# Performance work log

Measured on AMD Instinct MI355X. Metric: run time of the kernel, lower is better.

The kernel has to match this reference:

```python
import jax, jax.numpy as jnp
import numpy as np

EPS = 1e-5  # torch BatchNorm1d default eps

def _bn(x, g, b, m, v):
    # eval-mode BatchNorm1d with running statistics
    return (x - m) * jax.lax.rsqrt(v + EPS) * g + b

def setup_inputs() -> dict:
    key = jax.random.key(0)
    ks = jax.random.split(key, 6)
    N, E, D = 10000, 320000, 128
    h = jax.random.normal(ks[0], (N, D), dtype=jnp.float32)
    src = jax.random.randint(ks[1], (E,), 0, N)
    dst = jax.random.randint(ks[2], (E,), 0, N)
    # Linear weights (torch layout: [out, in]), kaiming-ish scale
    W0 = jax.random.normal(ks[3], (128, 256), dtype=jnp.float32) * (1.0 / np.sqrt(256))
    b0 = jnp.zeros((128,), jnp.float32)
    W1 = jax.random.normal(ks[4], (128, 128), dtype=jnp.float32) * (1.0 / np.sqrt(128))
    b1 = jnp.zeros((128,), jnp.float32)
    W2 = jax.random.normal(ks[5], (1, 128), dtype=jnp.float32) * (1.0 / np.sqrt(128))
    b2 = jnp.zeros((1,), jnp.float32)
    # BatchNorm affine params + running stats per layer input size
    g0, be0, m0, v0 = jnp.ones((256,)), jnp.zeros((256,)), jnp.zeros((256,)), jnp.ones((256,))
    g1, be1, m1, v1 = jnp.ones((128,)), jnp.zeros((128,)), jnp.zeros((128,)), jnp.ones((128,))
    g2, be2, m2, v2 = jnp.ones((128,)), jnp.zeros((128,)), jnp.zeros((128,)), jnp.ones((128,))
    return dict(h=h, src=src, dst=dst, W0=W0, b0=b0, W1=W1, b1=b1, W2=W2, b2=b2,
                g0=g0, be0=be0, g1=g1, be1=be1, g2=g2, be2=be2,
                m0=m0, v0=v0, m1=m1, v1=v1, m2=m2, v2=v2)

def reference(h, src, dst, W0, b0, W1, b1, W2, b2,
              g0, be0, g1, be1, g2, be2, m0, v0, m1, v1, m2, v2):
    # edge gather + concat: [E, 2*D]
    x = jnp.concatenate([h[src], h[dst]], axis=1)
    # stage 0: BN -> Linear (dropout is identity in eval)
    x = _bn(x, g0, be0, m0, v0) @ W0.T + b0
    # stage 1: ReLU -> BN -> Linear
    x = jax.nn.relu(x)
    x = _bn(x, g1, be1, m1, v1) @ W1.T + b1
    # stage 2: ReLU -> BN -> Linear
    x = jax.nn.relu(x)
    x = _bn(x, g2, be2, m2, v2) @ W2.T + b2
    return x  # [E, 1] edge scores
```

## Files before the change

kernel.cpp:

```cpp
#include <hip/hip_runtime.h>
#include <hip/hip_bf16.h>

#define BN_EPS 1e-5f
#define MG 2
#define GEDGES 32

typedef short bf16x8 __attribute__((ext_vector_type(8)));
typedef float f32x4  __attribute__((ext_vector_type(4)));

static __device__ __forceinline__ unsigned short f2bf(float f) {
    union { float f; unsigned int u; } v; v.f = f;
    unsigned int u = v.u;
    unsigned int r = (u + 0x7FFFu + ((u >> 16) & 1u)) >> 16;
    return (unsigned short)r;
}

static __device__ __forceinline__ unsigned short f2bf_hw(float f) {
    __hip_bfloat16 b = __float2bfloat16(f);
    union { __hip_bfloat16 b; unsigned short u; } v; v.b = b;
    return v.u;
}

static __device__ __forceinline__ unsigned short f2h(float f) {
    union { _Float16 h; unsigned short u; } v; v.h = (_Float16)f;
    return v.u;
}

static __device__ __forceinline__ float h2f(short s) {
    union { short s; _Float16 h; } v; v.s = s;
    return (float)v.h;
}

__global__ __launch_bounds__(256) void k_prep(
        const float* __restrict__ h, unsigned short* __restrict__ hb, int n4, int nCvt,
        const float* __restrict__ W0, const float* __restrict__ b0,
        const float* __restrict__ W1, const float* __restrict__ b1,
        const float* __restrict__ W2, const float* __restrict__ b2,
        const float* __restrict__ g0, const float* __restrict__ be0,
        const float* __restrict__ m0, const float* __restrict__ v0,
        const float* __restrict__ g1, const float* __restrict__ be1,
        const float* __restrict__ m1, const float* __restrict__ v1,
        const float* __restrict__ g2, const float* __restrict__ be2,
        const float* __restrict__ m2, const float* __restrict__ v2,
        unsigned short* __restrict__ W0sw, unsigned short* __restrict__ W1sw,
        float* __restrict__ b0f, float* __restrict__ b1f,
        float* __restrict__ w2f, float* __restrict__ b2f) {
    const int b = blockIdx.x;
    const int tid = threadIdx.x;

    if (b < nCvt) {
        int i = b * 256 + tid;
        if (i < n4) {
            float4 f = ((const float4*)h)[i];
            ushort4 o;
            o.x = f2bf(f.x); o.y = f2bf(f.y); o.z = f2bf(f.z); o.w = f2bf(f.w);
            ((ushort4*)hb)[i] = o;
        }
        return;
    }
    int br = b - nCvt;
    if (br < 128) {
        int t = br * 256 + tid;
        int j = t & 7, lane = (t >> 3) & 63, nt = (t >> 9) & 7, kb = t >> 12;
        int k = kb * 32 + (lane >> 4) * 8 + j;
        int n = nt * 16 + (lane & 15);
        float s = g0[k] * rsqrtf(v0[k] + BN_EPS);
        W0sw[t] = f2bf(W0[n * 256 + k] * s);
        return;
    }
    br -= 128;
    if (br < 64) {
        int t = br * 256 + tid;
        int j = t & 7, lane = (t >> 3) & 63, nt = (t >> 9) & 7, kb = t >> 12;
        int k = kb * 32 + (lane >> 4) * 8 + j;
        int n = nt * 16 + (lane & 15);
        float s = g1[k] * rsqrtf(v1[k] + BN_EPS);
        W1sw[t] = f2bf(W1[n * 128 + k] * s);
        return;
    }
    br -= 64;
    {
        if (tid >= 64) return;
        const int i = br, lane = tid;
        float s0 = 0.f;
#pragma unroll
        for (int c = 0; c < 4; c++) {
            int k = c * 64 + lane;
            float sc = g0[k] * rsqrtf(v0[k] + BN_EPS);
            s0 += W0[i * 256 + k] * (be0[k] - m0[k] * sc);
        }
        float s1 = 0.f;
#pragma unroll
        for (int c = 0; c < 2; c++) {
            int k = c * 64 + lane;
            float sc = g1[k] * rsqrtf(v1[k] + BN_EPS);
            s1 += W1[i * 128 + k] * (be1[k] - m1[k] * sc);
        }
        float s2 = 0.f;
        if (i == 0) {
#pragma unroll
            for (int c = 0; c < 2; c++) {
                int k = c * 64 + lane;
                float sc = g2[k] * rsqrtf(v2[k] + BN_EPS);
                s2 += W2[k] * (be2[k] - m2[k] * sc);
            }
        }
#pragma unroll
        for (int off = 1; off < 64; off <<= 1) {
            s0 += __shfl_xor(s0, off);
            s1 += __shfl_xor(s1, off);
            s2 += __shfl_xor(s2, off);
        }
        if (lane == 0) {
            b0f[i] = b0[i] + s0;
            b1f[i] = b1[i] + s1;
            w2f[i] = W2[i] * (g2[i] * rsqrtf(v2[i] + BN_EPS));
            if (i == 0) b2f[0] = b2[0] + s2;
        }
    }
}

__global__ __launch_bounds__(256) void k_node(
        const float* __restrict__ h,
        const unsigned short* __restrict__ W0sw,
        const float* __restrict__ b0f,
        unsigned short* __restrict__ UV, int N) {
    const int tid  = threadIdx.x;
    const int wave = tid >> 6;
    const int lane = tid & 63;
    const int quad = lane >> 4;
    const int m    = lane & 15;
    const int nb   = blockIdx.x * 32;

    bf16x8 B0[8][2];
#pragma unroll
    for (int kb = 0; kb < 8; kb++)
#pragma unroll
        for (int hh = 0; hh < 2; hh++)
            B0[kb][hh] = *(const bf16x8*)(W0sw + ((kb * 8 + (wave * 2 + hh)) * 64 + lane) * 8);

    float b0v[2];
#pragma unroll
    for (int hh = 0; hh < 2; hh++) b0v[hh] = b0f[(wave * 2 + hh) * 16 + m];

    f32x4 au[MG][2], av[MG][2];
#pragma unroll
    for (int g = 0; g < MG; g++)
#pragma unroll
        for (int hh = 0; hh < 2; hh++) {
            au[g][hh] = (f32x4){0.f, 0.f, 0.f, 0.f};
            av[g][hh] = (f32x4){0.f, 0.f, 0.f, 0.f};
        }

#pragma unroll
    for (int g = 0; g < MG; g++) {
        int nrow = nb + g * 16 + m; if (nrow >= N) nrow = N - 1;
        const float* hrow = h + (size_t)nrow * 128;
#pragma unroll
        for (int kb = 0; kb < 4; kb++) {
            const float* hp = hrow + kb * 32 + quad * 8;
            f32x4 f0 = *(const f32x4*)hp;
            f32x4 f1 = *(const f32x4*)(hp + 4);
            bf16x8 a;
            a[0] = (short)f2bf_hw(f0[0]); a[1] = (short)f2bf_hw(f0[1]);
            a[2] = (short)f2bf_hw(f0[2]); a[3] = (short)f2bf_hw(f0[3]);
            a[4] = (short)f2bf_hw(f1[0]); a[5] = (short)f2bf_hw(f1[1]);
            a[6] = (short)f2bf_hw(f1[2]); a[7] = (short)f2bf_hw(f1[3]);
#pragma unroll
            for (int hh = 0; hh < 2; hh++) {
                au[g][hh] = __builtin_amdgcn_mfma_f32_16x16x32_bf16(a, B0[kb][hh],     au[g][hh], 0, 0, 0);
                av[g][hh] = __builtin_amdgcn_mfma_f32_16x16x32_bf16(a, B0[kb + 4][hh], av[g][hh], 0, 0, 0);
            }
        }
    }

#pragma unroll
    for (int g = 0; g < MG; g++)
#pragma unroll
        for (int hh = 0; hh < 2; hh++) {
            int col = (wave * 2 + hh) * 16 + m;
#pragma unroll
            for (int r = 0; r < 4; r++) {
                int node = nb + g * 16 + quad * 4 + r;
                if (node < N) {
                    UV[(size_t)node * 256 + col]       = f2h(au[g][hh][r] + b0v[hh]);
                    UV[(size_t)node * 256 + 128 + col] = f2h(av[g][hh][r]);
                }
            }
        }
}

__global__ __launch_bounds__(256, 3) void k_main_uv(
        const int* __restrict__ src, const int* __restrict__ dst,
        const unsigned short* __restrict__ UV,
        const unsigned short* __restrict__ W1sw,
        const float* __restrict__ b1f, const float* __restrict__ w2f,
        const float* __restrict__ b2fp,
        float* __restrict__ out, int E, int nGroups) {
    __shared__ __align__(16) unsigned short x1S[2][MG][4][64][8];
    __shared__ float pS[2][4][GEDGES];

    const int tid  = threadIdx.x;
    const int wave = tid >> 6;
    const int lane = tid & 63;
    const int quad = lane >> 4;
    const int m    = lane & 15;
    const int es   = tid >> 3;
    const int fc   = tid & 7;

    bf16x8 B1[4][2];
#pragma unroll
    for (int kb = 0; kb < 4; kb++)
#pragma unroll
        for (int hh = 0; hh < 2; hh++)
            B1[kb][hh] = *(const bf16x8*)(W1sw + ((kb * 8 + (wave * 2 + hh)) * 64 + lane) * 8);

    float b1v[2], w2v[2];
#pragma unroll
    for (int hh = 0; hh < 2; hh++) {
        int n = (wave * 2 + hh) * 16 + m;
        b1v[hh] = b1f[n];
        w2v[hh] = w2f[n];
    }
    const float b2s = *b2fp;
    const int stride = gridDim.x;

    int gi = blockIdx.x;
    int p = 0;
    int eM1 = -1, eM2 = -1;
    bf16x8 uA, uB, vA, vB;

    {
        int e = gi * GEDGES + es; if (e >= E) e = E - 1;
        int rs_ = src[e], rd_ = dst[e];
        const bf16x8* up = (const bf16x8*)(UV + (size_t)rs_ * 256 + fc * 16);
        const bf16x8* vp = (const bf16x8*)(UV + (size_t)rd_ * 256 + 128 + fc * 16);
        uA = up[0]; uB = up[1]; vA = vp[0]; vB = vp[1];
    }

    for (; gi < nGroups; gi += stride, p ^= 1) {
        __syncthreads();

        if (eM2 >= 0 && wave == 0 && lane < GEDGES) {
            int e = eM2 + lane;
            if (e < E)
                out[e] = pS[p ^ 1][0][lane] + pS[p ^ 1][1][lane] +
                         pS[p ^ 1][2][lane] + pS[p ^ 1][3][lane] + b2s;
        }

        {
            bf16x8 w0, w1;
#pragma unroll
            for (int j = 0; j < 8; j++) {
                float s0 = h2f(uA[j]) + h2f(vA[j]);
                float s1 = h2f(uB[j]) + h2f(vB[j]);
                s0 = s0 > 0.f ? s0 : 0.f;
                s1 = s1 > 0.f ? s1 : 0.f;
                w0[j] = (short)f2bf_hw(s0);
                w1[j] = (short)f2bf_hw(s1);
            }
            int g = es >> 4, s15 = es & 15, kb = fc >> 1, q0 = (fc & 1) * 2;
            *(bf16x8*)&x1S[p][g][kb][q0 * 16 + s15][0]       = w0;
            *(bf16x8*)&x1S[p][g][kb][(q0 + 1) * 16 + s15][0] = w1;
        }

        {
            int gN = gi + stride;
            int ebN = (gN < nGroups ? gN : gi) * GEDGES;
            int e = ebN + es; if (e >= E) e = E - 1;
            int rs_ = src[e], rd_ = dst[e];
            const bf16x8* up = (const bf16x8*)(UV + (size_t)rs_ * 256 + fc * 16);
            const bf16x8* vp = (const bf16x8*)(UV + (size_t)rd_ * 256 + 128 + fc * 16);
            uA = up[0]; uB = up[1]; vA = vp[0]; vB = vp[1];
        }

        if (eM1 >= 0) {
            f32x4 acc1[MG][2];
#pragma unroll
            for (int g = 0; g < MG; g++)
#pragma unroll
                for (int hh = 0; hh < 2; hh++) acc1[g][hh] = (f32x4){0.f, 0.f, 0.f, 0.f};

#pragma unroll
            for (int kb = 0; kb < 4; kb++) {
                bf16x8 a1[MG];
#pragma unroll
                for (int g = 0; g < MG; g++)
                    a1[g] = *(const bf16x8*)&x1S[p ^ 1][g][kb][lane][0];
#pragma unroll
                for (int hh = 0; hh < 2; hh++)
#pragma unroll
                    for (int g = 0; g < MG; g++)
                        acc1[g][hh] = __builtin_amdgcn_mfma_f32_16x16x32_bf16(a1[g], B1[kb][hh], acc1[g][hh], 0, 0, 0);
            }

#pragma unroll
            for (int g = 0; g < MG; g++) {
                float s[4] = {0.f, 0.f, 0.f, 0.f};
#pragma unroll
                for (int hh = 0; hh < 2; hh++)
#pragma unroll
                    for (int r = 0; r < 4; r++) {
                        float v = acc1[g][hh][r] + b1v[hh];
                        v = v > 0.f ? v : 0.f;
                        s[r] += v * w2v[hh];
                    }
#pragma unroll
                for (int off = 1; off < 16; off <<= 1)
#pragma unroll
                    for (int r = 0; r < 4; r++) s[r] += __shfl_xor(s[r], off, 16);
                if (m == 0) {
#pragma unroll
                    for (int r = 0; r < 4; r++)
                        pS[p][wave][g * 16 + quad * 4 + r] = s[r];
                }
            }
        }

        eM2 = eM1;
        eM1 = gi * GEDGES;
    }

    __syncthreads();
    if (eM2 >= 0 && wave == 0 && lane < GEDGES) {
        int e = eM2 + lane;
        if (e < E)
            out[e] = pS[p ^ 1][0][lane] + pS[p ^ 1][1][lane] +
                     pS[p ^ 1][2][lane] + pS[p ^ 1][3][lane] + b2s;
    }
    if (eM1 >= 0) {
        f32x4 acc1[MG][2];
#pragma unroll
        for (int g = 0; g < MG; g++)
#pragma unroll
            for (int hh = 0; hh < 2; hh++) acc1[g][hh] = (f32x4){0.f, 0.f, 0.f, 0.f};
#pragma unroll
        for (int kb = 0; kb < 4; kb++) {
            bf16x8 a1[MG];
#pragma unroll
            for (int g = 0; g < MG; g++)
                a1[g] = *(const bf16x8*)&x1S[p ^ 1][g][kb][lane][0];
#pragma unroll
            for (int hh = 0; hh < 2; hh++)
#pragma unroll
                for (int g = 0; g < MG; g++)
                    acc1[g][hh] = __builtin_amdgcn_mfma_f32_16x16x32_bf16(a1[g], B1[kb][hh], acc1[g][hh], 0, 0, 0);
        }
#pragma unroll
        for (int g = 0; g < MG; g++) {
            float s[4] = {0.f, 0.f, 0.f, 0.f};
#pragma unroll
            for (int hh = 0; hh < 2; hh++)
#pragma unroll
                for (int r = 0; r < 4; r++) {
                    float v = acc1[g][hh][r] + b1v[hh];
                    v = v > 0.f ? v : 0.f;
                    s[r] += v * w2v[hh];
                }
#pragma unroll
            for (int off = 1; off < 16; off <<= 1)
#pragma unroll
                for (int r = 0; r < 4; r++) s[r] += __shfl_xor(s[r], off, 16);
            if (m == 0) {
#pragma unroll
                for (int r = 0; r < 4; r++)
                    pS[p][wave][g * 16 + quad * 4 + r] = s[r];
            }
        }
    }
    __syncthreads();
    if (eM1 >= 0 && wave == 0 && lane < GEDGES) {
        int e = eM1 + lane;
        if (e < E)
            out[e] = pS[p][0][lane] + pS[p][1][lane] +
                     pS[p][2][lane] + pS[p][3][lane] + b2s;
    }
}

static __device__ __forceinline__ void dma_issue(
        unsigned short* AbufBase, const unsigned short* __restrict__ hb,
        int gOwn, int halfOwn, int lane, int quad, int row) {
#pragma unroll
    for (int kb4 = 0; kb4 < 4; kb4++) {
        const unsigned short* gp = hb + (size_t)row * 128 + kb4 * 32 + quad * 8;
        unsigned short* lp = AbufBase + ((gOwn * 2 + halfOwn) * 4 + kb4) * 512 + lane * 8;
        __builtin_amdgcn_global_load_lds(
            (const __attribute__((address_space(1))) void*)gp,
            (__attribute__((address_space(3))) void*)lp, 16, 0, 0);
    }
}

__global__ __launch_bounds__(256, 3) void k_main_gather(
        const int* __restrict__ src, const int* __restrict__ dst,
        const unsigned short* __restrict__ hb,
        const unsigned short* __restrict__ W0sw, const unsigned short* __restrict__ W1sw,
        const float* __restrict__ b0f, const float* __restrict__ b1f,
        const float* __restrict__ w2f, const float* __restrict__ b2fp,
        float* __restrict__ out, int E, int nGroups) {
    __shared__ __align__(16) unsigned short Abuf[2][MG * 2 * 4 * 64 * 8];
    __shared__ __align__(16) unsigned short x1S[2][MG][4][64][8];
    __shared__ float pS[2][4][GEDGES];

    const int tid  = threadIdx.x;
    const int wave = tid >> 6;
    const int lane = tid & 63;
    const int quad = lane >> 4;
    const int m    = lane & 15;

    bf16x8 B0[8][2], B1[4][2];
#pragma unroll
    for (int kb = 0; kb < 8; kb++)
#pragma unroll
        for (int hh = 0; hh < 2; hh++)
            B0[kb][hh] = *(const bf16x8*)(W0sw + ((kb * 8 + (wave * 2 + hh)) * 64 + lane) * 8);
#pragma unroll
    for (int kb = 0; kb < 4; kb++)
#pragma unroll
        for (int hh = 0; hh < 2; hh++)
            B1[kb][hh] = *(const bf16x8*)(W1sw + ((kb * 8 + (wave * 2 + hh)) * 64 + lane) * 8);

    float b0v[2], b1v[2], w2v[2];
#pragma unroll
    for (int hh = 0; hh < 2; hh++) {
        int n = (wave * 2 + hh) * 16 + m;
        b0v[hh] = b0f[n];
        b1v[hh] = b1f[n];
        w2v[hh] = w2f[n];
    }
    const float b2s = *b2fp;
    const int stride = gridDim.x;

    const int gOwn = wave >> 1;
    const int halfOwn = wave & 1;
    const int* __restrict__ idxP = halfOwn ? dst : src;

    int gi = blockIdx.x;
    int p = 0;
    int eM1 = -1, eM2 = -1;
    int rN;

    {
        int e = gi * GEDGES + gOwn * 16 + m; if (e >= E) e = E - 1;
        int r0 = idxP[e];
        dma_issue(&Abuf[0][0], hb, gOwn, halfOwn, lane, quad, r0);
        int gN = gi + stride;
        int ebN = (gN < nGroups ? gN : gi) * GEDGES;
        int eN = ebN + gOwn * 16 + m; if (eN >= E) eN = E - 1;
        rN = idxP[eN];
    }

    for (; gi < nGroups; gi += stride, p ^= 1) {
        __syncthreads();

        if (eM2 >= 0 && wave == 0 && lane < GEDGES) {
            int e = eM2 + lane;
            if (e < E)
                out[e] = pS[p ^ 1][0][lane] + pS[p ^ 1][1][lane] +
                         pS[p ^ 1][2][lane] + pS[p ^ 1][3][lane] + b2s;
        }

        if (gi + stride < nGroups)
            dma_issue(&Abuf[p ^ 1][0], hb, gOwn, halfOwn, lane, quad, rN);

        {
            int g2i = gi + 2 * stride;
            int eb2 = (g2i < nGroups ? g2i : gi) * GEDGES;
            int e2 = eb2 + gOwn * 16 + m; if (e2 >= E) e2 = E - 1;
            rN = idxP[e2];
        }

        {
            f32x4 acc0[MG][2];
#pragma unroll
            for (int g = 0; g < MG; g++)
#pragma unroll
                for (int hh = 0; hh < 2; hh++) acc0[g][hh] = (f32x4){0.f, 0.f, 0.f, 0.f};

#pragma unroll
            for (int kb = 0; kb < 8; kb++) {
                bf16x8 a[MG];
#pragma unroll
                for (int g = 0; g < MG; g++)
                    a[g] = *(const bf16x8*)(&Abuf[p][((g * 2 + (kb >> 2)) * 4 + (kb & 3)) * 512 + lane * 8]);
#pragma unroll
                for (int hh = 0; hh < 2; hh++)
#pragma unroll
                    for (int g = 0; g < MG; g++)
                        acc0[g][hh] = __builtin_amdgcn_mfma_f32_16x16x32_bf16(a[g], B0[kb][hh], acc0[g][hh], 0, 0, 0);
            }
#pragma unroll
            for (int g = 0; g < MG; g++) {
#pragma unroll
                for (int hh = 0; hh < 2; hh++) {
                    int qp = (hh << 1) | (m >> 3);
                    int j  = m & 7;
#pragma unroll
                    for (int r = 0; r < 4; r++) {
                        float v = acc0[g][hh][r] + b0v[hh];
                        v = v > 0.f ? v : 0.f;
                        x1S[p][g][wave][qp * 16 + quad * 4 + r][j] = f2bf_hw(v);
                    }
                }
            }
        }

        if (eM1 >= 0) {
            f32x4 acc1[MG][2];
#pragma unroll
            for (int g = 0; g < MG; g++)
#pragma unroll
                for (int hh = 0; hh < 2; hh++) acc1[g][hh] = (f32x4){0.f, 0.f, 0.f, 0.f};

#pragma unroll
            for (int kb = 0; kb < 4; kb++) {
                bf16x8 a1[MG];
#pragma unroll
                for (int g = 0; g < MG; g++)
                    a1[g] = *(const bf16x8*)&x1S[p ^ 1][g][kb][lane][0];
#pragma unroll
                for (int hh = 0; hh < 2; hh++)
#pragma unroll
                    for (int g = 0; g < MG; g++)
                        acc1[g][hh] = __builtin_amdgcn_mfma_f32_16x16x32_bf16(a1[g], B1[kb][hh], acc1[g][hh], 0, 0, 0);
            }
#pragma unroll
            for (int g = 0; g < MG; g++) {
                float s[4] = {0.f, 0.f, 0.f, 0.f};
#pragma unroll
                for (int hh = 0; hh < 2; hh++)
#pragma unroll
                    for (int r = 0; r < 4; r++) {
                        float v = acc1[g][hh][r] + b1v[hh];
                        v = v > 0.f ? v : 0.f;
                        s[r] += v * w2v[hh];
                    }
#pragma unroll
                for (int off = 1; off < 16; off <<= 1)
#pragma unroll
                    for (int r = 0; r < 4; r++) s[r] += __shfl_xor(s[r], off, 16);
                if (m == 0) {
#pragma unroll
                    for (int r = 0; r < 4; r++)
                        pS[p][wave][g * 16 + quad * 4 + r] = s[r];
                }
            }
        }

        eM2 = eM1;
        eM1 = gi * GEDGES;
    }

    __syncthreads();
    if (eM2 >= 0 && wave == 0 && lane < GEDGES) {
        int e = eM2 + lane;
        if (e < E)
            out[e] = pS[p ^ 1][0][lane] + pS[p ^ 1][1][lane] +
                     pS[p ^ 1][2][lane] + pS[p ^ 1][3][lane] + b2s;
    }
    if (eM1 >= 0) {
        f32x4 acc1[MG][2];
#pragma unroll
        for (int g = 0; g < MG; g++)
#pragma unroll
            for (int hh = 0; hh < 2; hh++) acc1[g][hh] = (f32x4){0.f, 0.f, 0.f, 0.f};
#pragma unroll
        for (int kb = 0; kb < 4; kb++) {
            bf16x8 a1[MG];
#pragma unroll
            for (int g = 0; g < MG; g++)
                a1[g] = *(const bf16x8*)&x1S[p ^ 1][g][kb][lane][0];
#pragma unroll
            for (int hh = 0; hh < 2; hh++)
#pragma unroll
                for (int g = 0; g < MG; g++)
                    acc1[g][hh] = __builtin_amdgcn_mfma_f32_16x16x32_bf16(a1[g], B1[kb][hh], acc1[g][hh], 0, 0, 0);
        }
#pragma unroll
        for (int g = 0; g < MG; g++) {
            float s[4] = {0.f, 0.f, 0.f, 0.f};
#pragma unroll
            for (int hh = 0; hh < 2; hh++)
#pragma unroll
                for (int r = 0; r < 4; r++) {
                    float v = acc1[g][hh][r] + b1v[hh];
                    v = v > 0.f ? v : 0.f;
                    s[r] += v * w2v[hh];
                }
#pragma unroll
            for (int off = 1; off < 16; off <<= 1)
#pragma unroll
                for (int r = 0; r < 4; r++) s[r] += __shfl_xor(s[r], off, 16);
            if (m == 0) {
#pragma unroll
                for (int r = 0; r < 4; r++)
                    pS[p][wave][g * 16 + quad * 4 + r] = s[r];
            }
        }
    }
    __syncthreads();
    if (eM1 >= 0 && wave == 0 && lane < GEDGES) {
        int e = eM1 + lane;
        if (e < E)
            out[e] = pS[p][0][lane] + pS[p][1][lane] +
                     pS[p][2][lane] + pS[p][3][lane] + b2s;
    }
}

extern "C" void kernel_launch(void* const* d_in, const int* in_sizes, int n_in,
                              void* d_out, int out_size, void* d_ws, size_t ws_size,
                              hipStream_t stream) {
    const float* h   = (const float*)d_in[0];
    const int*   src = (const int*)d_in[1];
    const int*   dst = (const int*)d_in[2];
    const float* W0  = (const float*)d_in[3];
    const float* b0  = (const float*)d_in[4];
    const float* W1  = (const float*)d_in[5];
    const float* b1  = (const float*)d_in[6];
    const float* W2  = (const float*)d_in[7];
    const float* b2  = (const float*)d_in[8];
    const float* g0  = (const float*)d_in[9];
    const float* be0 = (const float*)d_in[10];
    const float* g1  = (const float*)d_in[11];
    const float* be1 = (const float*)d_in[12];
    const float* g2  = (const float*)d_in[13];
    const float* be2 = (const float*)d_in[14];
    const float* m0  = (const float*)d_in[15];
    const float* v0  = (const float*)d_in[16];
    const float* m1  = (const float*)d_in[17];
    const float* v1  = (const float*)d_in[18];
    const float* m2  = (const float*)d_in[19];
    const float* v2  = (const float*)d_in[20];
    float* out = (float*)d_out;

    const int hsz = in_sizes[0];
    const int E   = in_sizes[1];
    const int N   = hsz / 128;
    const int nGroups = (E + GEDGES - 1) / GEDGES;

    const size_t TAIL = 65536 + 32768 + 512 + 512 + 512 + 16;
    size_t uvBytes = ((size_t)N * 256 * 2 + 255) & ~(size_t)255;
    size_t needA   = uvBytes + TAIL;

    char* ws = (char*)d_ws;

    if (ws_size >= needA) {
        size_t off = uvBytes;
        unsigned short* UV   = (unsigned short*)ws;
        unsigned short* W0sw = (unsigned short*)(ws + off);  off += 65536;
        unsigned short* W1sw = (unsigned short*)(ws + off);  off += 32768;
        float* b0f = (float*)(ws + off);  off += 512;
        float* b1f = (float*)(ws + off);  off += 512;
        float* w2f = (float*)(ws + off);  off += 512;
        float* b2f = (float*)(ws + off);  off += 16;

        k_prep<<<320, 256, 0, stream>>>(h, nullptr, 0, 0,
                                        W0, b0, W1, b1, W2, b2,
                                        g0, be0, m0, v0, g1, be1, m1, v1,
                                        g2, be2, m2, v2,
                                        W0sw, W1sw, b0f, b1f, w2f, b2f);
        int nodeBlocks = (N + 31) / 32;
        k_node<<<nodeBlocks, 256, 0, stream>>>(h, W0sw, b0f, UV, N);
        int nBlocks = nGroups < 768 ? nGroups : 768;
        k_main_uv<<<nBlocks, 256, 0, stream>>>(src, dst, UV, W1sw,
                                               b1f, w2f, b2f, out, E, nGroups);
    } else {
        size_t off = (size_t)hsz * 2;
        off = (off + 255) & ~(size_t)255;
        unsigned short* hb   = (unsigned short*)ws;
        unsigned short* W0sw = (unsigned short*)(ws + off);  off += 65536;
        unsigned short* W1sw = (unsigned short*)(ws + off);  off += 32768;
        float* b0f = (float*)(ws + off);  off += 512;
        float* b1f = (float*)(ws + off);  off += 512;
        float* w2f = (float*)(ws + off);  off += 512;
        float* b2f = (float*)(ws + off);  off += 16;

        int n4   = hsz / 4;
        int nCvt = (n4 + 255) / 256;
        int prepBlocks = nCvt + 128 + 64 + 128;
        k_prep<<<prepBlocks, 256, 0, stream>>>(h, hb, n4, nCvt,
                                               W0, b0, W1, b1, W2, b2,
                                               g0, be0, m0, v0, g1, be1, m1, v1,
                                               g2, be2, m2, v2,
                                               W0sw, W1sw, b0f, b1f, w2f, b2f);
        int nBlocks = nGroups < 768 ? nGroups : 768;
        k_main_gather<<<nBlocks, 256, 0, stream>>>(src, dst, hb, W0sw, W1sw,
                                                   b0f, b1f, w2f, b2f, out, E, nGroups);
    }
}
```

Before: 141.5 us.

## Prefetch edge indices two groups ahead, swizzle LDS tile, raise occupancy

Measured after the change: 135.4 us. 1.05x faster.

```diff
diff --git a/kernel.cpp b/kernel.cpp
--- a/kernel.cpp
+++ b/kernel.cpp
@@ -29,6 +29,11 @@
 static __device__ __forceinline__ float h2f(short s) {
     union { short s; _Float16 h; } v; v.s = s;
     return (float)v.h;
+}
+
+static __device__ __forceinline__ unsigned short* x1_ptr(unsigned short* base, int g, int kb, int row) {
+    int off = g * 4096 + (kb * 1024 + (((row * 16)) ^ (kb << 5)));
+    return (unsigned short*)((char*)base + off);
 }
 
 __global__ __launch_bounds__(256) void k_prep(
@@ -190,7 +195,7 @@
         }
 }
 
-__global__ __launch_bounds__(256, 3) void k_main_uv(
+__global__ __launch_bounds__(256, 4) void k_main_uv(
         const int* __restrict__ src, const int* __restrict__ dst,
         const unsigned short* __restrict__ UV,
         const unsigned short* __restrict__ W1sw,
@@ -229,24 +234,22 @@
     int p = 0;
     int eM1 = -1, eM2 = -1;
     bf16x8 uA, uB, vA, vB;
+    int rsC, rdC;
+    int rsN, rdN;
 
     {
-        int e = gi * GEDGES + es; if (e >= E) e = E - 1;
-        int rs_ = src[e], rd_ = dst[e];
-        const bf16x8* up = (const bf16x8*)(UV + (size_t)rs_ * 256 + fc * 16);
-        const bf16x8* vp = (const bf16x8*)(UV + (size_t)rd_ * 256 + 128 + fc * 16);
+        int e0 = gi * GEDGES + es; if (e0 >= E) e0 = E - 1;
+        int rs0 = src[e0], rd0 = dst[e0];
+        const bf16x8* up = (const bf16x8*)(UV + (size_t)rs0 * 256 + fc * 16);
+        const bf16x8* vp = (const bf16x8*)(UV + (size_t)rd0 * 256 + 128 + fc * 16);
         uA = up[0]; uB = up[1]; vA = vp[0]; vB = vp[1];
+        int g1 = gi + stride;
+        int e1 = (g1 < nGroups ? g1 : gi) * GEDGES + es; if (e1 >= E) e1 = E - 1;
+        rsC = src[e1]; rdC = dst[e1];
     }
 
     for (; gi < nGroups; gi += stride, p ^= 1) {
         __syncthreads();
-
-        if (eM2 >= 0 && wave == 0 && lane < GEDGES) {
-            int e = eM2 + lane;
-            if (e < E)
-                out[e] = pS[p ^ 1][0][lane] + pS[p ^ 1][1][lane] +
-                         pS[p ^ 1][2][lane] + pS[p ^ 1][3][lane] + b2s;
-        }
 
         {
             bf16x8 w0, w1;
@@ -260,18 +263,28 @@
                 w1[j] = (short)f2bf_hw(s1);
             }
             int g = es >> 4, s15 = es & 15, kb = fc >> 1, q0 = (fc & 1) * 2;
-            *(bf16x8*)&x1S[p][g][kb][q0 * 16 + s15][0]       = w0;
-            *(bf16x8*)&x1S[p][g][kb][(q0 + 1) * 16 + s15][0] = w1;
+            unsigned short* bw = &x1S[p][0][0][0][0];
+            *(bf16x8*)x1_ptr(bw, g, kb, q0 * 16 + s15)       = w0;
+            *(bf16x8*)x1_ptr(bw, g, kb, (q0 + 1) * 16 + s15) = w1;
         }
 
         {
-            int gN = gi + stride;
-            int ebN = (gN < nGroups ? gN : gi) * GEDGES;
-            int e = ebN + es; if (e >= E) e = E - 1;
-            int rs_ = src[e], rd_ = dst[e];
-            const bf16x8* up = (const bf16x8*)(UV + (size_t)rs_ * 256 + fc * 16);
-            const bf16x8* vp = (const bf16x8*)(UV + (size_t)rd_ * 256 + 128 + fc * 16);
+            const bf16x8* up = (const bf16x8*)(UV + (size_t)rsC * 256 + fc * 16);
+            const bf16x8* vp = (const bf16x8*)(UV + (size_t)rdC * 256 + 128 + fc * 16);
             uA = up[0]; uB = up[1]; vA = vp[0]; vB = vp[1];
+        }
+
+        {
+            int gN2 = gi + 2 * stride;
+            int e2 = (gN2 < nGroups ? gN2 : gi) * GEDGES + es; if (e2 >= E) e2 = E - 1;
+            rsN = src[e2]; rdN = dst[e2];
+        }
+
+        if (eM2 >= 0 && wave == 0 && lane < GEDGES) {
+            int e = eM2 + lane;
+            if (e < E)
+                out[e] = pS[p ^ 1][0][lane] + pS[p ^ 1][1][lane] +
+                         pS[p ^ 1][2][lane] + pS[p ^ 1][3][lane] + b2s;
         }
 
         if (eM1 >= 0) {
@@ -281,12 +294,13 @@
 #pragma unroll
                 for (int hh = 0; hh < 2; hh++) acc1[g][hh] = (f32x4){0.f, 0.f, 0.f, 0.f};
 
+            unsigned short* brd = &x1S[p ^ 1][0][0][0][0];
 #pragma unroll
             for (int kb = 0; kb < 4; kb++) {
                 bf16x8 a1[MG];
 #pragma unroll
                 for (int g = 0; g < MG; g++)
-                    a1[g] = *(const bf16x8*)&x1S[p ^ 1][g][kb][lane][0];
+                    a1[g] = *(const bf16x8*)x1_ptr(brd, g, kb, lane);
 #pragma unroll
                 for (int hh = 0; hh < 2; hh++)
 #pragma unroll
@@ -319,6 +333,7 @@
 
         eM2 = eM1;
         eM1 = gi * GEDGES;
+        rsC = rsN; rdC = rdN;
     }
 
     __syncthreads();
@@ -334,12 +349,13 @@
         for (int g = 0; g < MG; g++)
 #pragma unroll
             for (int hh = 0; hh < 2; hh++) acc1[g][hh] = (f32x4){0.f, 0.f, 0.f, 0.f};
+        unsigned short* brd = &x1S[p ^ 1][0][0][0][0];
 #pragma unroll
         for (int kb = 0; kb < 4; kb++) {
             bf16x8 a1[MG];
 #pragma unroll
             for (int g = 0; g < MG; g++)
-                a1[g] = *(const bf16x8*)&x1S[p ^ 1][g][kb][lane][0];
+                a1[g] = *(const bf16x8*)x1_ptr(brd, g, kb, lane);
 #pragma unroll
             for (int hh = 0; hh < 2; hh++)
 #pragma unroll
@@ -660,7 +676,7 @@
                                         W0sw, W1sw, b0f, b1f, w2f, b2f);
         int nodeBlocks = (N + 31) / 32;
         k_node<<<nodeBlocks, 256, 0, stream>>>(h, W0sw, b0f, UV, N);
-        int nBlocks = nGroups < 768 ? nGroups : 768;
+        int nBlocks = nGroups < 1024 ? nGroups : 1024;
         k_main_uv<<<nBlocks, 256, 0, stream>>>(src, dst, UV, W1sw,
                                                b1f, w2f, b2f, out, E, nGroups);
     } else {
```
